# Kernel optimization log

Hardware: AMD Instinct MI355X
Metric: run time of the kernel (lower is better)

## Reference

```python
import jax, jax.numpy as jnp
import numpy as np

# FreqEncoder constants (from init_kwargs)
X_DIM = 3
MIN_DEG = 0.0
MAX_DEG = 8.0
NUM_SCALES = 8            # max_deg - min_deg
RES = 128                 # 2 ** log2_res
NUM_CH = 8                # num_feats (channels per grid)
STD = 0.001
P = 262144                # number of sample points


def setup_inputs() -> dict:
    key = jax.random.key(0)
    k1, k2 = jax.random.split(key)
    x = jax.random.uniform(k1, (P, X_DIM), dtype=jnp.float32)
    # learned 1D grids: [num_scales*2*x_dim, num_channels, res]
    features = jax.random.normal(k2, (NUM_SCALES * 2 * X_DIM, NUM_CH, RES), dtype=jnp.float32) * STD
    return {"x": x, "features": features}


def reference(x, features):
    S, D, C, res = NUM_SCALES, X_DIM, NUM_CH, RES
    N = S * 2 * D  # number of 1D grids
    p = x.shape[0]

    # scales = 2 ** linspace(min_deg, max_deg, num_scales)  (matches torch.linspace)
    scales = 2.0 ** jnp.linspace(MIN_DEG, MAX_DEG, S).astype(x.dtype)  # [S]

    xb = x[:, None, :] * scales[None, :, None]                     # [P, S, D]
    latent = jnp.sin(jnp.stack([xb, xb + 0.5 * jnp.pi], axis=-2))  # [P, S, 2, D]

    # values in [-1, 1] used as grid_sample y-coords; one grid per (s, phase, d)
    v = latent.reshape(p, N).T                                     # [N, P]

    # align_corners=True bilinear unnormalization along the res axis
    pos = (v + 1.0) * 0.5 * (res - 1)                              # [N, P] in [0, res-1]
    i0f = jnp.floor(pos)
    frac = pos - i0f                                               # [N, P]
    i0 = jnp.clip(i0f, 0, res - 1).astype(jnp.int32)
    i1 = jnp.clip(i0 + 1, 0, res - 1)

    idx0 = jnp.broadcast_to(i0[:, None, :], (N, C, p))
    idx1 = jnp.broadcast_to(i1[:, None, :], (N, C, p))
    f0 = jnp.take_along_axis(features, idx0, axis=2)               # [N, C, P]
    f1 = jnp.take_along_axis(features, idx1, axis=2)               # [N, C, P]
    fs = f0 * (1.0 - frac[:, None, :]) + f1 * frac[:, None, :]     # [N, C, P]

    # [N, C, P] -> [S, 2, D, C, P] -> [P, C, S, 2, D], add residual, flatten
    fs = fs.reshape(S, 2, D, C, p).transpose(4, 3, 0, 1, 2)
    out = (fs + latent[:, None, :, :, :]).reshape(p, C * S * 2 * D)

    # use_identity=True: prepend raw coordinates
    return jnp.concatenate([x, out], axis=-1)                      # [P, 3 + 384]
```

## Files before the change

kernel.cpp:

```cpp
#include <hip/hip_runtime.h>
#include <hip/hip_bf16.h>
#include <stdint.h>


constexpr int P_PTS = 262144;
constexpr int S_SC  = 8;
constexpr int D_DIM = 3;
constexpr int C_CH  = 8;
constexpr int RES   = 128;
constexpr int N_GR  = S_SC * 2 * D_DIM;
constexpr int OW    = 3 + C_CH * N_GR;
constexpr int KPB   = 16;
constexpr int BLK   = 256;

constexpr float ENC_SCALE = 256.0f;
constexpr float DEC_SCALE = 1.0f / 256.0f;
constexpr float INV_2PI   = 0.15915494309189535f;

typedef float f32x2 __attribute__((ext_vector_type(2)));

__device__ uint4 g_pair[N_GR * RES];

__global__ __launch_bounds__(256) void feat_pack_kernel(const float* __restrict__ f) {
    int t = blockIdx.x * 256 + threadIdx.x;
    if (t >= N_GR * RES) return;
    int n = t / RES, i = t % RES;
    int ia = i;
    int ib = min(i + 1, RES - 1);

    uint32_t d[4];
    {
        float a = f[(n * C_CH + 0) * RES + ia] * ENC_SCALE;
        float b = f[(n * C_CH + 1) * RES + ia] * ENC_SCALE;
        float c = f[(n * C_CH + 2) * RES + ia] * ENC_SCALE;
        float e = f[(n * C_CH + 3) * RES + ia] * ENC_SCALE;
        int lo = __builtin_amdgcn_cvt_pk_fp8_f32(a, b, 0, false);
        d[0] = (uint32_t)__builtin_amdgcn_cvt_pk_fp8_f32(c, e, lo, true);
    }
    {
        float a = f[(n * C_CH + 4) * RES + ia] * ENC_SCALE;
        float b = f[(n * C_CH + 5) * RES + ia] * ENC_SCALE;
        float c = f[(n * C_CH + 6) * RES + ia] * ENC_SCALE;
        float e = f[(n * C_CH + 7) * RES + ia] * ENC_SCALE;
        int lo = __builtin_amdgcn_cvt_pk_fp8_f32(a, b, 0, false);
        d[1] = (uint32_t)__builtin_amdgcn_cvt_pk_fp8_f32(c, e, lo, true);
    }
    {
        float a = f[(n * C_CH + 0) * RES + ib] * ENC_SCALE;
        float b = f[(n * C_CH + 1) * RES + ib] * ENC_SCALE;
        float c = f[(n * C_CH + 2) * RES + ib] * ENC_SCALE;
        float e = f[(n * C_CH + 3) * RES + ib] * ENC_SCALE;
        int lo = __builtin_amdgcn_cvt_pk_fp8_f32(a, b, 0, false);
        d[2] = (uint32_t)__builtin_amdgcn_cvt_pk_fp8_f32(c, e, lo, true);
    }
    {
        float a = f[(n * C_CH + 4) * RES + ib] * ENC_SCALE;
        float b = f[(n * C_CH + 5) * RES + ib] * ENC_SCALE;
        float c = f[(n * C_CH + 6) * RES + ib] * ENC_SCALE;
        float e = f[(n * C_CH + 7) * RES + ib] * ENC_SCALE;
        int lo = __builtin_amdgcn_cvt_pk_fp8_f32(a, b, 0, false);
        d[3] = (uint32_t)__builtin_amdgcn_cvt_pk_fp8_f32(c, e, lo, true);
    }
    g_pair[t] = make_uint4(d[0], d[1], d[2], d[3]);
}

__global__ __launch_bounds__(256) void freq_encode_kernel(const float* __restrict__ x,
                                                          float* __restrict__ out) {
    __shared__ float s_out[KPB * OW];
    __shared__ float s_x[KPB * D_DIM];

    const int tid = threadIdx.x;
    const int p0  = blockIdx.x * KPB;

    if (tid < KPB * D_DIM) {
        float v = x[(size_t)p0 * D_DIM + tid];
        s_x[tid] = v;
        int pl = tid / D_DIM, d = tid % D_DIM;
        s_out[pl * OW + d] = v;
    }
    __syncthreads();

    #pragma unroll
    for (int it = 0; it < 3; ++it) {
        int t  = tid + it * BLK;
        int pl = t / N_GR;
        int n  = t % N_GR;
        int s  = n / (2 * D_DIM);
        int r  = n % (2 * D_DIM);
        int ph = r / D_DIM;
        int d  = r % D_DIM;

        float xv    = s_x[pl * D_DIM + d];
        float scale = exp2f((float)s * (8.0f / 7.0f));
        float rv  = fmaf(xv * scale, INV_2PI, ph ? 0.25f : 0.0f);
        float rev = __builtin_amdgcn_fractf(rv);
        float lat = __builtin_amdgcn_sinf(rev);

        float pos  = (lat + 1.0f) * 63.5f;
        float i0f  = floorf(pos);
        float frac = pos - i0f;
        int   i0   = (int)i0f;
        i0 = max(0, min(i0, RES - 1));

        uint4 pk = g_pair[n * RES + i0];

        f32x2 a01 = __builtin_amdgcn_cvt_pk_f32_fp8(pk.x, false);
        f32x2 a23 = __builtin_amdgcn_cvt_pk_f32_fp8(pk.x, true);
        f32x2 a45 = __builtin_amdgcn_cvt_pk_f32_fp8(pk.y, false);
        f32x2 a67 = __builtin_amdgcn_cvt_pk_f32_fp8(pk.y, true);
        f32x2 b01 = __builtin_amdgcn_cvt_pk_f32_fp8(pk.z, false);
        f32x2 b23 = __builtin_amdgcn_cvt_pk_f32_fp8(pk.z, true);
        f32x2 b45 = __builtin_amdgcn_cvt_pk_f32_fp8(pk.w, false);
        f32x2 b67 = __builtin_amdgcn_cvt_pk_f32_fp8(pk.w, true);

        float omd = (1.0f - frac) * DEC_SCALE;
        float frd = frac * DEC_SCALE;

        float* dst = &s_out[pl * OW + 3 + n];
        dst[0 * N_GR] = fmaf(a01[0], omd, fmaf(b01[0], frd, lat));
        dst[1 * N_GR] = fmaf(a01[1], omd, fmaf(b01[1], frd, lat));
        dst[2 * N_GR] = fmaf(a23[0], omd, fmaf(b23[0], frd, lat));
        dst[3 * N_GR] = fmaf(a23[1], omd, fmaf(b23[1], frd, lat));
        dst[4 * N_GR] = fmaf(a45[0], omd, fmaf(b45[0], frd, lat));
        dst[5 * N_GR] = fmaf(a45[1], omd, fmaf(b45[1], frd, lat));
        dst[6 * N_GR] = fmaf(a67[0], omd, fmaf(b67[0], frd, lat));
        dst[7 * N_GR] = fmaf(a67[1], omd, fmaf(b67[1], frd, lat));
    }
    __syncthreads();

    constexpr int NV = KPB * OW / 4;
    const float4* src = reinterpret_cast<const float4*>(s_out);
    float4*       dst = reinterpret_cast<float4*>(out + (size_t)p0 * OW);
    for (int i = tid; i < NV; i += BLK) {
        dst[i] = src[i];
    }
}

extern "C" void kernel_launch(void* const* d_in, const int* in_sizes, int n_in,
                              void* d_out, int out_size, void* d_ws, size_t ws_size,
                              hipStream_t stream) {
    const float* x    = (const float*)d_in[0];
    const float* feat = (const float*)d_in[1];
    float*       out  = (float*)d_out;

    int n_pairs = N_GR * RES;
    feat_pack_kernel<<<(n_pairs + 255) / 256, 256, 0, stream>>>(feat);

    freq_encode_kernel<<<P_PTS / KPB, BLK, 0, stream>>>(x, out);
}
```

Before: 109.2 us.

## Stage packed feature table in LDS and loop over point chunks per block

Each 1024-thread block copies the whole packed fp8 pair table (about 96 KB) into LDS once, then processes 8 chunks of 32 points, looking up features in LDS instead of global memory. The aim is to replace scattered global/L2 gathers with LDS lookups and spread the table-load cost over more points per block. In exchange, about 147 KB of dynamic LDS limits each CU to one resident block. Chunks are separated by barriers, so the LDS staging of one chunk cannot overlap the global store of the previous one. The 1536 work items per chunk also map unevenly onto 1024 threads, and a dynamic LDS request above 64 KB may need an explicit attribute to launch.

```diff
diff --git a/kernel.cpp b/kernel.cpp
--- a/kernel.cpp
+++ b/kernel.cpp
@@ -10,12 +10,19 @@
 constexpr int RES   = 128;
 constexpr int N_GR  = S_SC * 2 * D_DIM;
 constexpr int OW    = 3 + C_CH * N_GR;
-constexpr int KPB   = 16;
-constexpr int BLK   = 256;
+constexpr int KPB   = 32;
+constexpr int CHUNKS = 8;
+constexpr int PPB   = KPB * CHUNKS;
+constexpr int BLK   = 1024;
 
 constexpr float ENC_SCALE = 256.0f;
 constexpr float DEC_SCALE = 1.0f / 256.0f;
 constexpr float INV_2PI   = 0.15915494309189535f;
+
+constexpr int LDS_TABLE_B = N_GR * RES * 16;
+constexpr int LDS_SOUT_B  = KPB * OW * 4;
+constexpr int LDS_SX_B    = PPB * D_DIM * 4;
+constexpr int LDS_TOTAL_B = LDS_TABLE_B + LDS_SOUT_B + LDS_SX_B;
 
 typedef float f32x2 __attribute__((ext_vector_type(2)));
 
@@ -64,75 +71,79 @@
     g_pair[t] = make_uint4(d[0], d[1], d[2], d[3]);
 }
 
-__global__ __launch_bounds__(256) void freq_encode_kernel(const float* __restrict__ x,
-                                                          float* __restrict__ out) {
-    __shared__ float s_out[KPB * OW];
-    __shared__ float s_x[KPB * D_DIM];
+__global__ __launch_bounds__(1024) void freq_encode_kernel(const float* __restrict__ x,
+                                                           float* __restrict__ out) {
+    extern __shared__ char smem[];
+    uint4* ld_pair = reinterpret_cast<uint4*>(smem);
+    float* s_out   = reinterpret_cast<float*>(smem + LDS_TABLE_B);
+    float* s_x     = reinterpret_cast<float*>(smem + LDS_TABLE_B + LDS_SOUT_B);
 
-    const int tid = threadIdx.x;
-    const int p0  = blockIdx.x * KPB;
+    const int tid   = threadIdx.x;
+    const int pbase = blockIdx.x * PPB;
 
-    if (tid < KPB * D_DIM) {
-        float v = x[(size_t)p0 * D_DIM + tid];
-        s_x[tid] = v;
-        int pl = tid / D_DIM, d = tid % D_DIM;
-        s_out[pl * OW + d] = v;
-    }
+    for (int i = tid; i < N_GR * RES; i += BLK) ld_pair[i] = g_pair[i];
+    for (int i = tid; i < PPB * D_DIM; i += BLK) s_x[i] = x[(size_t)pbase * D_DIM + i];
     __syncthreads();
 
-    #pragma unroll
-    for (int it = 0; it < 3; ++it) {
-        int t  = tid + it * BLK;
-        int pl = t / N_GR;
-        int n  = t % N_GR;
-        int s  = n / (2 * D_DIM);
-        int r  = n % (2 * D_DIM);
-        int ph = r / D_DIM;
-        int d  = r % D_DIM;
+    for (int ch = 0; ch < CHUNKS; ++ch) {
+        const int p0l = ch * KPB;
 
-        float xv    = s_x[pl * D_DIM + d];
-        float scale = exp2f((float)s * (8.0f / 7.0f));
-        float rv  = fmaf(xv * scale, INV_2PI, ph ? 0.25f : 0.0f);
-        float rev = __builtin_amdgcn_fractf(rv);
-        float lat = __builtin_amdgcn_sinf(rev);
+        if (tid < KPB * D_DIM) {
+            s_out[(tid / D_DIM) * OW + (tid % D_DIM)] = s_x[p0l * D_DIM + tid];
+        }
 
-        float pos  = (lat + 1.0f) * 63.5f;
-        float i0f  = floorf(pos);
-        float frac = pos - i0f;
-        int   i0   = (int)i0f;
-        i0 = max(0, min(i0, RES - 1));
+        for (int u = tid; u < KPB * N_GR; u += BLK) {
+            int pl = u / N_GR;
+            int n  = u % N_GR;
+            int s  = n / (2 * D_DIM);
+            int r  = n % (2 * D_DIM);
+            int ph = r / D_DIM;
+            int d  = r % D_DIM;
 
-        uint4 pk = g_pair[n * RES + i0];
+            float xv    = s_x[(p0l + pl) * D_DIM + d];
+            float scale = exp2f((float)s * (8.0f / 7.0f));
+            float rv    = fmaf(xv * scale, INV_2PI, ph ? 0.25f : 0.0f);
+            float lat   = __builtin_amdgcn_sinf(__builtin_amdgcn_fractf(rv));
 
-        f32x2 a01 = __builtin_amdgcn_cvt_pk_f32_fp8(pk.x, false);
-        f32x2 a23 = __builtin_amdgcn_cvt_pk_f32_fp8(pk.x, true);
-        f32x2 a45 = __builtin_amdgcn_cvt_pk_f32_fp8(pk.y, false);
-        f32x2 a67 = __builtin_amdgcn_cvt_pk_f32_fp8(pk.y, true);
-        f32x2 b01 = __builtin_amdgcn_cvt_pk_f32_fp8(pk.z, false);
-        f32x2 b23 = __builtin_amdgcn_cvt_pk_f32_fp8(pk.z, true);
-        f32x2 b45 = __builtin_amdgcn_cvt_pk_f32_fp8(pk.w, false);
-        f32x2 b67 = __builtin_amdgcn_cvt_pk_f32_fp8(pk.w, true);
+            float pos  = (lat + 1.0f) * 63.5f;
+            float i0f  = floorf(pos);
+            float frac = pos - i0f;
+            int   i0   = (int)i0f;
+            i0 = max(0, min(i0, RES - 1));
 
-        float omd = (1.0f - frac) * DEC_SCALE;
-        float frd = frac * DEC_SCALE;
+            uint4 pk = ld_pair[n * RES + i0];
 
-        float* dst = &s_out[pl * OW + 3 + n];
-        dst[0 * N_GR] = fmaf(a01[0], omd, fmaf(b01[0], frd, lat));
-        dst[1 * N_GR] = fmaf(a01[1], omd, fmaf(b01[1], frd, lat));
-        dst[2 * N_GR] = fmaf(a23[0], omd, fmaf(b23[0], frd, lat));
-        dst[3 * N_GR] = fmaf(a23[1], omd, fmaf(b23[1], frd, lat));
-        dst[4 * N_GR] = fmaf(a45[0], omd, fmaf(b45[0], frd, lat));
-        dst[5 * N_GR] = fmaf(a45[1], omd, fmaf(b45[1], frd, lat));
-        dst[6 * N_GR] = fmaf(a67[0], omd, fmaf(b67[0], frd, lat));
-        dst[7 * N_GR] = fmaf(a67[1], omd, fmaf(b67[1], frd, lat));
-    }
-    __syncthreads();
+            f32x2 a01 = __builtin_amdgcn_cvt_pk_f32_fp8(pk.x, false);
+            f32x2 a23 = __builtin_amdgcn_cvt_pk_f32_fp8(pk.x, true);
+            f32x2 a45 = __builtin_amdgcn_cvt_pk_f32_fp8(pk.y, false);
+            f32x2 a67 = __builtin_amdgcn_cvt_pk_f32_fp8(pk.y, true);
+            f32x2 b01 = __builtin_amdgcn_cvt_pk_f32_fp8(pk.z, false);
+            f32x2 b23 = __builtin_amdgcn_cvt_pk_f32_fp8(pk.z, true);
+            f32x2 b45 = __builtin_amdgcn_cvt_pk_f32_fp8(pk.w, false);
+            f32x2 b67 = __builtin_amdgcn_cvt_pk_f32_fp8(pk.w, true);
 
-    constexpr int NV = KPB * OW / 4;
-    const float4* src = reinterpret_cast<const float4*>(s_out);
-    float4*       dst = reinterpret_cast<float4*>(out + (size_t)p0 * OW);
-    for (int i = tid; i < NV; i += BLK) {
-        dst[i] = src[i];
+            float omd = (1.0f - frac) * DEC_SCALE;
+            float frd = frac * DEC_SCALE;
+
+            float* dst = &s_out[pl * OW + 3 + n];
+            dst[0 * N_GR] = fmaf(a01[0], omd, fmaf(b01[0], frd, lat));
+            dst[1 * N_GR] = fmaf(a01[1], omd, fmaf(b01[1], frd, lat));
+            dst[2 * N_GR] = fmaf(a23[0], omd, fmaf(b23[0], frd, lat));
+            dst[3 * N_GR] = fmaf(a23[1], omd, fmaf(b23[1], frd, lat));
+            dst[4 * N_GR] = fmaf(a45[0], omd, fmaf(b45[0], frd, lat));
+            dst[5 * N_GR] = fmaf(a45[1], omd, fmaf(b45[1], frd, lat));
+            dst[6 * N_GR] = fmaf(a67[0], omd, fmaf(b67[0], frd, lat));
+            dst[7 * N_GR] = fmaf(a67[1], omd, fmaf(b67[1], frd, lat));
+        }
+        __syncthreads();
+
+        constexpr int NV = KPB * OW / 4;
+        const float4* src = reinterpret_cast<const float4*>(s_out);
+        float4*       dst = reinterpret_cast<float4*>(out + ((size_t)pbase + p0l) * OW);
+        for (int i = tid; i < NV; i += BLK) {
+            dst[i] = src[i];
+        }
+        __syncthreads();
     }
 }
 
@@ -146,5 +157,5 @@
     int n_pairs = N_GR * RES;
     feat_pack_kernel<<<(n_pairs + 255) / 256, 256, 0, stream>>>(feat);
 
-    freq_encode_kernel<<<P_PTS / KPB, BLK, 0, stream>>>(x, out);
+    freq_encode_kernel<<<P_PTS / PPB, BLK, LDS_TOTAL_B, stream>>>(x, out);
 }
```

Result: faster. 88.80 us (-18.7%).
